# Kernel optimization log

Measured on AMD Instinct MI355X. Metric: run time of the kernel, lower is better.

Reference implementation:

```python
import jax, jax.numpy as jnp
import numpy as np

B, N, D = 2, 256, 512
H = 4 * D  # mlp_hidden_dim


def setup_inputs() -> dict:
    key = jax.random.key(0)
    ks = jax.random.split(key, 14)
    s_in = 1.0 / np.sqrt(D)
    s_h = 1.0 / np.sqrt(H)
    s_cat = 1.0 / np.sqrt(2 * D)
    return {
        "x_v": jax.random.normal(ks[0], (B, N, D), jnp.float32),
        "x_a": jax.random.normal(ks[1], (B, N, D), jnp.float32),
        # weights stored as (in, out); y = x @ W + b (same math as torch Linear)
        "W1v": jax.random.uniform(ks[2], (D, H), jnp.float32, -s_in, s_in),
        "b1v": jax.random.uniform(ks[3], (H,), jnp.float32, -s_in, s_in),
        "W1a": jax.random.uniform(ks[4], (D, H), jnp.float32, -s_in, s_in),
        "b1a": jax.random.uniform(ks[5], (H,), jnp.float32, -s_in, s_in),
        "Wmv": jax.random.uniform(ks[6], (H, D), jnp.float32, -s_h, s_h),
        "bmv": jax.random.uniform(ks[7], (D,), jnp.float32, -s_h, s_h),
        "Wma": jax.random.uniform(ks[8], (H, D), jnp.float32, -s_h, s_h),
        "bma": jax.random.uniform(ks[9], (D,), jnp.float32, -s_h, s_h),
        "Wout": jax.random.uniform(ks[10], (2 * D, D), jnp.float32, -s_cat, s_cat),
        "bout": jax.random.uniform(ks[11], (D,), jnp.float32, -s_cat, s_cat),
    }


def reference(x_v, x_a, W1v, b1v, W1a, b1a, Wmv, bmv, Wma, bma, Wout, bout):
    # pairwise Manhattan distance: [B, N, M]
    dist = jnp.sum(jnp.abs(x_v[:, :, None, :] - x_a[:, None, :, :]), axis=-1)
    dv = dist.mean(axis=2)  # [B, N] mean distance of each v-token to all a-tokens
    da = dist.mean(axis=1)  # [B, M]
    xv_w = x_v * dv[..., None]
    xa_w = x_a * da[..., None]
    # dropout prob = 0.0 -> identity
    hv = jax.nn.gelu(xv_w @ W1v + b1v, approximate=False) @ Wmv + bmv
    ha = jax.nn.gelu(xa_w @ W1a + b1a, approximate=False) @ Wma + bma
    combined = jnp.concatenate([hv, ha], axis=-1)  # [B, N, 2D]
    return combined @ Wout + bout
```

## Files before the change

kernel.cpp:

```cpp
#include <hip/hip_runtime.h>
#include <math.h>

#define Bsz  2
#define Ntok 256
#define Ddim 512
#define Hdim 2048
#define Mrows 512

typedef __bf16 bf16_8 __attribute__((ext_vector_type(8)));
typedef __bf16 bf16_4 __attribute__((ext_vector_type(4)));
typedef float  f32x4_t __attribute__((ext_vector_type(4)));

struct PrepPtrs {
    const float* src[3];
    __bf16*      dst[3];
    const float* xv;
    const float* xa;
    float*       pv;
    float*       pa;
    float*       out;
    float*       bc;
};

__global__ __launch_bounds__(256) void prep_kernel(PrepPtrs p) {
    __shared__ float tile[64][65];
    __shared__ float red[4][4];

    int blk = blockIdx.x;
    int tid = threadIdx.x;

    if (blk < 640) {
        const int Ks[3]  = {512, 512, 1024};
        const int Ns[3]  = {2048, 2048, 512};
        const int off[4] = {0, 256, 512, 640};
        int mi = 0;
        while (blk >= off[mi + 1]) ++mi;
        int local = blk - off[mi];
        int shift = (mi < 2) ? 5 : 3;
        int bx = local & ((1 << shift) - 1);
        int by = local >> shift;
        const float* src = p.src[mi];
        __bf16*      dst = p.dst[mi];
        int K = Ks[mi], N = Ns[mi];
        int n0 = bx << 6, k0 = by << 6;

        int klb = tid >> 4, nl = (tid & 15) << 2;
#pragma unroll
        for (int pass = 0; pass < 4; ++pass) {
            int kl = (pass << 4) + klb;
            float4 v = *(const float4*)&src[(size_t)(k0 + kl) * N + n0 + nl];
            tile[kl][nl + 0] = v.x;
            tile[kl][nl + 1] = v.y;
            tile[kl][nl + 2] = v.z;
            tile[kl][nl + 3] = v.w;
        }
        __syncthreads();
        int nl2 = tid >> 2, kb = (tid & 3) << 2;
#pragma unroll
        for (int pass = 0; pass < 4; ++pass) {
            int kl2 = (pass << 4) + kb;
            bf16_4 o;
#pragma unroll
            for (int i = 0; i < 4; ++i) o[i] = (__bf16)tile[kl2 + i][nl2];
            *(bf16_4*)&dst[(size_t)(n0 + nl2) * K + k0 + kl2] = o;
        }
    } else if (blk < 1664) {
        int bx   = blk - 640;
        int jc   = bx & 3;
        int g    = bx >> 2;
        int role = g >> 7;
        int b    = (g >> 6) & 1;
        int i0   = (g & 63) << 2;
        const float* Q    = role ? p.xa : p.xv;
        const float* S    = role ? p.xv : p.xa;
        float*       outp = role ? p.pa : p.pv;

        int d0 = tid << 1;
        const float* Qb = Q + ((size_t)b * Ntok + i0) * Ddim + d0;
        const float* Sb = S + ((size_t)b * Ntok + (jc << 6)) * Ddim + d0;

        float2 q[4];
#pragma unroll
        for (int r = 0; r < 4; ++r) q[r] = *(const float2*)(Qb + r * Ddim);

        float acc[4] = {0.f, 0.f, 0.f, 0.f};
#pragma unroll 4
        for (int j = 0; j < 64; ++j) {
            float2 s = *(const float2*)(Sb + (size_t)j * Ddim);
#pragma unroll
            for (int r = 0; r < 4; ++r)
                acc[r] += fabsf(q[r].x - s.x) + fabsf(q[r].y - s.y);
        }
        int lane = tid & 63, wv = tid >> 6;
#pragma unroll
        for (int r = 0; r < 4; ++r) {
            float v = acc[r];
#pragma unroll
            for (int off2 = 32; off2; off2 >>= 1) v += __shfl_down(v, off2);
            if (lane == 0) red[wv][r] = v;
        }
        __syncthreads();
        if (tid < 4) {
            float v = red[0][tid] + red[1][tid] + red[2][tid] + red[3][tid];
            outp[jc * Mrows + b * Ntok + i0 + tid] = v;
        }
    } else {
        int zb = blk - 1664;
        float4 z4 = {0.f, 0.f, 0.f, 0.f};
        *(float4*)&p.out[((size_t)zb * 256 + tid) * 4] = z4;
        if (zb == 0 && tid < 128) *(float4*)&p.bc[tid * 4] = z4;
    }
}

template <int GELU, int AMODE, int BFP32, int OUTM>
__device__ void gemm_tile(__bf16 (&As)[2][64][40], __bf16 (&Bs)[2][64][40],
                          const void* Aa, int lda, const void* Bv, int ldb,
                          const float* bias, const float* scale4,
                          void* C, int ldc, int Kdim,
                          int m0, int n0, int addBias) {
    const int tid = threadIdx.x;
    const int row = tid >> 2;
    const int kc  = (tid & 3) << 3;

    const __bf16* Bb  = (const __bf16*)Bv + (size_t)(n0 + row) * ldb + kc;
    const float*  Bf  = (const float*)Bv + (size_t)(n0 + row) * ldb + kc;
    const float*  Af  = (const float*)Aa + (size_t)(m0 + row) * lda + kc;
    const __bf16* Ab  = (const __bf16*)Aa + (size_t)(m0 + row) * lda + kc;
    float s = 1.0f;
    if (AMODE == 1) {
        int m = m0 + row;
        s = (scale4[m] + scale4[Mrows + m] + scale4[2 * Mrows + m] +
             scale4[3 * Mrows + m]) * (1.0f / 256.0f);
    }

    const int wave = tid >> 6, lane = tid & 63;
    const int moff = (wave >> 1) << 5, noff = (wave & 1) << 5;
    const int lrow = lane & 15, quad = lane >> 4;

    struct Stage {
        float4 aF0, aF1, bF0, bF1;
        bf16_8 a8, b8;
    };
    Stage sR, sN;

    auto loadStage = [&](int kt, Stage& st) {
        if (BFP32) {
            st.bF0 = *(const float4*)(Bf + kt);
            st.bF1 = *(const float4*)(Bf + kt + 4);
        } else {
            st.b8 = *(const bf16_8*)(Bb + kt);
        }
        if (AMODE == 1) {
            st.aF0 = *(const float4*)(Af + kt);
            st.aF1 = *(const float4*)(Af + kt + 4);
        } else {
            st.a8 = *(const bf16_8*)(Ab + kt);
        }
    };
    auto storeStage = [&](int buf, const Stage& st) {
        bf16_8 a8, b8;
        if (AMODE == 1) {
            a8[0] = (__bf16)(st.aF0.x * s); a8[1] = (__bf16)(st.aF0.y * s);
            a8[2] = (__bf16)(st.aF0.z * s); a8[3] = (__bf16)(st.aF0.w * s);
            a8[4] = (__bf16)(st.aF1.x * s); a8[5] = (__bf16)(st.aF1.y * s);
            a8[6] = (__bf16)(st.aF1.z * s); a8[7] = (__bf16)(st.aF1.w * s);
        } else {
            a8 = st.a8;
        }
        if (BFP32) {
            b8[0] = (__bf16)st.bF0.x; b8[1] = (__bf16)st.bF0.y;
            b8[2] = (__bf16)st.bF0.z; b8[3] = (__bf16)st.bF0.w;
            b8[4] = (__bf16)st.bF1.x; b8[5] = (__bf16)st.bF1.y;
            b8[6] = (__bf16)st.bF1.z; b8[7] = (__bf16)st.bF1.w;
        } else {
            b8 = st.b8;
        }
        *(bf16_8*)&As[buf][row][kc] = a8;
        *(bf16_8*)&Bs[buf][row][kc] = b8;
    };

    f32x4_t acc00 = {0.f, 0.f, 0.f, 0.f};
    f32x4_t acc01 = {0.f, 0.f, 0.f, 0.f};
    f32x4_t acc10 = {0.f, 0.f, 0.f, 0.f};
    f32x4_t acc11 = {0.f, 0.f, 0.f, 0.f};

    const int nIter = Kdim >> 5;

    loadStage(0, sR);
    storeStage(0, sR);
    if (nIter > 1) loadStage(32, sR);
    __syncthreads();

    for (int it = 0; it < nIter; ++it) {
        const int cur = it & 1;
        bf16_8 a0 = *(const bf16_8*)&As[cur][moff + lrow][quad << 3];
        bf16_8 a1 = *(const bf16_8*)&As[cur][moff + 16 + lrow][quad << 3];
        bf16_8 b0 = *(const bf16_8*)&Bs[cur][noff + lrow][quad << 3];
        bf16_8 b1 = *(const bf16_8*)&Bs[cur][noff + 16 + lrow][quad << 3];
        if (it + 2 < nIter) loadStage((it + 2) << 5, sN);
        acc00 = __builtin_amdgcn_mfma_f32_16x16x32_bf16(a0, b0, acc00, 0, 0, 0);
        acc01 = __builtin_amdgcn_mfma_f32_16x16x32_bf16(a0, b1, acc01, 0, 0, 0);
        acc10 = __builtin_amdgcn_mfma_f32_16x16x32_bf16(a1, b0, acc10, 0, 0, 0);
        acc11 = __builtin_amdgcn_mfma_f32_16x16x32_bf16(a1, b1, acc11, 0, 0, 0);
        if (it + 1 < nIter) {
            storeStage(cur ^ 1, sR);
            sR = sN;
            __syncthreads();
        }
    }

    f32x4_t accs[2][2] = {{acc00, acc01}, {acc10, acc11}};
#pragma unroll
    for (int ti = 0; ti < 2; ++ti) {
#pragma unroll
        for (int tj = 0; tj < 2; ++tj) {
            int colg = n0 + noff + (tj << 4) + lrow;
            float bv = addBias ? bias[colg] : 0.0f;
#pragma unroll
            for (int r = 0; r < 4; ++r) {
                int rowg = m0 + moff + (ti << 4) + (quad << 2) + r;
                float v = accs[ti][tj][r] + bv;
                if (GELU) v = 0.5f * v * (1.0f + erff(v * 0.70710678118654752f));
                if (OUTM == 1)
                    ((__bf16*)C)[(size_t)rowg * ldc + colg] = (__bf16)v;
                else
                    atomicAdd((float*)C + (size_t)rowg * ldc + colg, v);
            }
        }
    }
}

struct APtrs {
    const float*  x[2];
    const __bf16* WT1[2];
    const float*  b1[2];
    const float*  pd[2];
    __bf16*       g1[2];
    const __bf16* WTout;
    const float*  Wm[2];
    const float*  bm[2];
    const float*  Wout;
    const float*  bout;
    __bf16*       WcT[2];
    float*        bc;
};

__global__ __launch_bounds__(256) void kernelA(APtrs p) {
    __shared__ __align__(16) __bf16 As[2][64][40];
    __shared__ __align__(16) __bf16 Bs[2][64][40];
    int blk = blockIdx.x;
    if (blk < 512) {
        int z = blk >> 8, t = blk & 255;
        int mt = t >> 5, nt = t & 31;
        gemm_tile<1, 1, 0, 1>(As, Bs, p.x[z], Ddim, p.WT1[z], Ddim,
                              p.b1[z], p.pd[z], p.g1[z], Hdim, Ddim,
                              mt << 6, nt << 6, 1);
    } else if (blk < 1024) {
        int b2 = blk - 512;
        int z = b2 >> 8, t = b2 & 255;
        int mt = t >> 5, nt = t & 31;
        gemm_tile<0, 0, 1, 1>(As, Bs, p.WTout + z * 512, 2 * Ddim,
                              p.Wm[z], Ddim, nullptr, nullptr,
                              p.WcT[z], Hdim, Ddim, mt << 6, nt << 6, 0);
    } else {
        int kb = blk - 1024;
        int tid = threadIdx.x;
        float a0 = 0.f, a1 = 0.f, a2 = 0.f, a3 = 0.f;
#pragma unroll 4
        for (int kk = 0; kk < 128; kk += 2) {
            int k0 = (kb << 7) + kk, k1 = k0 + 1;
            float bk0 = (k0 < 512) ? p.bm[0][k0] : p.bm[1][k0 - 512];
            float bk1 = (k1 < 512) ? p.bm[0][k1] : p.bm[1][k1 - 512];
            a0 += bk0 * p.Wout[(size_t)k0 * Ddim + tid];
            a1 += bk0 * p.Wout[(size_t)k0 * Ddim + tid + 256];
            a2 += bk1 * p.Wout[(size_t)k1 * Ddim + tid];
            a3 += bk1 * p.Wout[(size_t)k1 * Ddim + tid + 256];
        }
        if (kb == 0) { a0 += p.bout[tid]; a1 += p.bout[tid + 256]; }
        atomicAdd(&p.bc[tid],       a0 + a2);
        atomicAdd(&p.bc[tid + 256], a1 + a3);
    }
}

struct BPtrs {
    const __bf16* g1[2];
    const __bf16* WcT[2];
    const float*  bc;
    float*        out;
};

__global__ __launch_bounds__(256) void kernelB(BPtrs p) {
    __shared__ __align__(16) __bf16 As[2][64][40];
    __shared__ __align__(16) __bf16 Bs[2][64][40];
    int nt = blockIdx.x & 7, mt = (blockIdx.x >> 3) & 7, kz = blockIdx.x >> 6;
    int z = kz >> 2, koff = (kz & 3) << 9;
    gemm_tile<0, 0, 0, 2>(As, Bs, p.g1[z] + koff, Hdim, p.WcT[z] + koff, Hdim,
                          p.bc, nullptr, p.out, Ddim, Ddim,
                          mt << 6, nt << 6, kz == 0);
}

extern "C" void kernel_launch(void* const* d_in, const int* in_sizes, int n_in,
                              void* d_out, int out_size, void* d_ws, size_t ws_size,
                              hipStream_t stream) {
    const float* x_v  = (const float*)d_in[0];
    const float* x_a  = (const float*)d_in[1];
    const float* W1v  = (const float*)d_in[2];
    const float* b1v  = (const float*)d_in[3];
    const float* W1a  = (const float*)d_in[4];
    const float* b1a  = (const float*)d_in[5];
    const float* Wmv  = (const float*)d_in[6];
    const float* bmv  = (const float*)d_in[7];
    const float* Wma  = (const float*)d_in[8];
    const float* bma  = (const float*)d_in[9];
    const float* Wout = (const float*)d_in[10];
    const float* bout = (const float*)d_in[11];
    float* out = (float*)d_out;

    char* w = (char*)d_ws;
    auto alloc = [&](size_t bytes) {
        char* r = w;
        w += (bytes + 255) & ~(size_t)255;
        return (void*)r;
    };
    float*    pv    = (float*)alloc(4 * Mrows * 4);
    float*    pa    = (float*)alloc(4 * Mrows * 4);
    float*    bc    = (float*)alloc(Ddim * 4);
    __bf16*   WT1v  = (__bf16*)alloc((size_t)Hdim * Ddim * 2);
    __bf16*   WT1a  = (__bf16*)alloc((size_t)Hdim * Ddim * 2);
    __bf16*   WTout = (__bf16*)alloc((size_t)Ddim * 2 * Ddim * 2);
    __bf16*   WcTv  = (__bf16*)alloc((size_t)Ddim * Hdim * 2);
    __bf16*   WcTa  = (__bf16*)alloc((size_t)Ddim * Hdim * 2);
    __bf16*   g1v   = (__bf16*)alloc((size_t)Mrows * Hdim * 2);
    __bf16*   g1a   = (__bf16*)alloc((size_t)Mrows * Hdim * 2);

    PrepPtrs pp;
    pp.src[0] = W1v;  pp.dst[0] = WT1v;
    pp.src[1] = W1a;  pp.dst[1] = WT1a;
    pp.src[2] = Wout; pp.dst[2] = WTout;
    pp.xv = x_v; pp.xa = x_a; pp.pv = pv; pp.pa = pa;
    pp.out = out; pp.bc = bc;
    prep_kernel<<<dim3(1920), dim3(256), 0, stream>>>(pp);

    APtrs ap;
    ap.x[0] = x_v; ap.x[1] = x_a;
    ap.WT1[0] = WT1v; ap.WT1[1] = WT1a;
    ap.b1[0] = b1v; ap.b1[1] = b1a;
    ap.pd[0] = pv; ap.pd[1] = pa;
    ap.g1[0] = g1v; ap.g1[1] = g1a;
    ap.WTout = WTout;
    ap.Wm[0] = Wmv; ap.Wm[1] = Wma;
    ap.bm[0] = bmv; ap.bm[1] = bma;
    ap.Wout = Wout; ap.bout = bout;
    ap.WcT[0] = WcTv; ap.WcT[1] = WcTa;
    ap.bc = bc;
    kernelA<<<dim3(1032), dim3(256), 0, stream>>>(ap);

    BPtrs bp;
    bp.g1[0] = g1v; bp.g1[1] = g1a;
    bp.WcT[0] = WcTv; bp.WcT[1] = WcTa;
    bp.bc = bc; bp.out = out;
    kernelB<<<dim3(512), dim3(256), 0, stream>>>(bp);
}
```

Before: 130.6 us.

## Pre-convert activations to bf16 in prep and move bias-combine into prep kernel

The distance blocks now also write bf16 copies of x_v and x_a, so the first GEMM in kernelA loads bf16 activations and rescales them in registers instead of loading fp32. The bias-combine computation (bm·Wout + bout) moves from kernelA into prep_kernel, and zeroing of out and bc moves to hipMemsetAsync calls. This halves the activation bytes read by the first GEMM and shortens kernelA, at the cost of an extra bf16 round-trip, two memset launches, and scaling applied after bf16 rounding. Prep must complete the bc atomics after the memset, which stream order guarantees.

Measured after the change: 129.0 us. Within noise of the previous version (-1.2%).

```diff
diff --git a/kernel.cpp b/kernel.cpp
--- a/kernel.cpp
+++ b/kernel.cpp
@@ -9,6 +9,7 @@
 
 typedef __bf16 bf16_8 __attribute__((ext_vector_type(8)));
 typedef __bf16 bf16_4 __attribute__((ext_vector_type(4)));
+typedef __bf16 bf16_2 __attribute__((ext_vector_type(2)));
 typedef float  f32x4_t __attribute__((ext_vector_type(4)));
 
 struct PrepPtrs {
@@ -16,9 +17,12 @@
     __bf16*      dst[3];
     const float* xv;
     const float* xa;
+    __bf16*      xbf[2];
     float*       pv;
     float*       pa;
-    float*       out;
+    const float* bm[2];
+    const float* Wout;
+    const float* bout;
     float*       bc;
 };
 
@@ -83,6 +87,17 @@
 #pragma unroll
         for (int r = 0; r < 4; ++r) q[r] = *(const float2*)(Qb + r * Ddim);
 
+        if (jc == 0) {
+            __bf16* xb = p.xbf[role];
+#pragma unroll
+            for (int r = 0; r < 4; ++r) {
+                bf16_2 o;
+                o[0] = (__bf16)q[r].x;
+                o[1] = (__bf16)q[r].y;
+                *(bf16_2*)&xb[((size_t)b * Ntok + i0 + r) * Ddim + d0] = o;
+            }
+        }
+
         float acc[4] = {0.f, 0.f, 0.f, 0.f};
 #pragma unroll 4
         for (int j = 0; j < 64; ++j) {
@@ -105,10 +120,21 @@
             outp[jc * Mrows + b * Ntok + i0 + tid] = v;
         }
     } else {
-        int zb = blk - 1664;
-        float4 z4 = {0.f, 0.f, 0.f, 0.f};
-        *(float4*)&p.out[((size_t)zb * 256 + tid) * 4] = z4;
-        if (zb == 0 && tid < 128) *(float4*)&p.bc[tid * 4] = z4;
+        int kb = blk - 1664;
+        float a0 = 0.f, a1 = 0.f, a2 = 0.f, a3 = 0.f;
+#pragma unroll 4
+        for (int kk = 0; kk < 128; kk += 2) {
+            int k0 = (kb << 7) + kk, k1 = k0 + 1;
+            float bk0 = (k0 < 512) ? p.bm[0][k0] : p.bm[1][k0 - 512];
+            float bk1 = (k1 < 512) ? p.bm[0][k1] : p.bm[1][k1 - 512];
+            a0 += bk0 * p.Wout[(size_t)k0 * Ddim + tid];
+            a1 += bk0 * p.Wout[(size_t)k0 * Ddim + tid + 256];
+            a2 += bk1 * p.Wout[(size_t)k1 * Ddim + tid];
+            a3 += bk1 * p.Wout[(size_t)k1 * Ddim + tid + 256];
+        }
+        if (kb == 0) { a0 += p.bout[tid]; a1 += p.bout[tid + 256]; }
+        atomicAdd(&p.bc[tid],       a0 + a2);
+        atomicAdd(&p.bc[tid + 256], a1 + a3);
     }
 }
 
@@ -127,7 +153,7 @@
     const float*  Af  = (const float*)Aa + (size_t)(m0 + row) * lda + kc;
     const __bf16* Ab  = (const __bf16*)Aa + (size_t)(m0 + row) * lda + kc;
     float s = 1.0f;
-    if (AMODE == 1) {
+    if (AMODE == 1 || AMODE == 3) {
         int m = m0 + row;
         s = (scale4[m] + scale4[Mrows + m] + scale4[2 * Mrows + m] +
              scale4[3 * Mrows + m]) * (1.0f / 256.0f);
@@ -164,6 +190,10 @@
             a8[2] = (__bf16)(st.aF0.z * s); a8[3] = (__bf16)(st.aF0.w * s);
             a8[4] = (__bf16)(st.aF1.x * s); a8[5] = (__bf16)(st.aF1.y * s);
             a8[6] = (__bf16)(st.aF1.z * s); a8[7] = (__bf16)(st.aF1.w * s);
+        } else if (AMODE == 3) {
+#pragma unroll
+            for (int i = 0; i < 8; ++i)
+                a8[i] = (__bf16)((float)st.a8[i] * s);
         } else {
             a8 = st.a8;
         }
@@ -231,18 +261,14 @@
 }
 
 struct APtrs {
-    const float*  x[2];
+    const __bf16* xbf[2];
     const __bf16* WT1[2];
     const float*  b1[2];
     const float*  pd[2];
     __bf16*       g1[2];
     const __bf16* WTout;
     const float*  Wm[2];
-    const float*  bm[2];
-    const float*  Wout;
-    const float*  bout;
     __bf16*       WcT[2];
-    float*        bc;
 };
 
 __global__ __launch_bounds__(256) void kernelA(APtrs p) {
@@ -252,33 +278,16 @@
     if (blk < 512) {
         int z = blk >> 8, t = blk & 255;
         int mt = t >> 5, nt = t & 31;
-        gemm_tile<1, 1, 0, 1>(As, Bs, p.x[z], Ddim, p.WT1[z], Ddim,
+        gemm_tile<1, 3, 0, 1>(As, Bs, p.xbf[z], Ddim, p.WT1[z], Ddim,
                               p.b1[z], p.pd[z], p.g1[z], Hdim, Ddim,
                               mt << 6, nt << 6, 1);
-    } else if (blk < 1024) {
+    } else {
         int b2 = blk - 512;
         int z = b2 >> 8, t = b2 & 255;
         int mt = t >> 5, nt = t & 31;
         gemm_tile<0, 0, 1, 1>(As, Bs, p.WTout + z * 512, 2 * Ddim,
                               p.Wm[z], Ddim, nullptr, nullptr,
                               p.WcT[z], Hdim, Ddim, mt << 6, nt << 6, 0);
-    } else {
-        int kb = blk - 1024;
-        int tid = threadIdx.x;
-        float a0 = 0.f, a1 = 0.f, a2 = 0.f, a3 = 0.f;
-#pragma unroll 4
-        for (int kk = 0; kk < 128; kk += 2) {
-            int k0 = (kb << 7) + kk, k1 = k0 + 1;
-            float bk0 = (k0 < 512) ? p.bm[0][k0] : p.bm[1][k0 - 512];
-            float bk1 = (k1 < 512) ? p.bm[0][k1] : p.bm[1][k1 - 512];
-            a0 += bk0 * p.Wout[(size_t)k0 * Ddim + tid];
-            a1 += bk0 * p.Wout[(size_t)k0 * Ddim + tid + 256];
-            a2 += bk1 * p.Wout[(size_t)k1 * Ddim + tid];
-            a3 += bk1 * p.Wout[(size_t)k1 * Ddim + tid + 256];
-        }
-        if (kb == 0) { a0 += p.bout[tid]; a1 += p.bout[tid + 256]; }
-        atomicAdd(&p.bc[tid],       a0 + a2);
-        atomicAdd(&p.bc[tid + 256], a1 + a3);
     }
 }
 
@@ -325,6 +334,8 @@
     float*    pv    = (float*)alloc(4 * Mrows * 4);
     float*    pa    = (float*)alloc(4 * Mrows * 4);
     float*    bc    = (float*)alloc(Ddim * 4);
+    __bf16*   xbfv  = (__bf16*)alloc((size_t)Mrows * Ddim * 2);
+    __bf16*   xbfa  = (__bf16*)alloc((size_t)Mrows * Ddim * 2);
     __bf16*   WT1v  = (__bf16*)alloc((size_t)Hdim * Ddim * 2);
     __bf16*   WT1a  = (__bf16*)alloc((size_t)Hdim * Ddim * 2);
     __bf16*   WTout = (__bf16*)alloc((size_t)Ddim * 2 * Ddim * 2);
@@ -333,27 +344,31 @@
     __bf16*   g1v   = (__bf16*)alloc((size_t)Mrows * Hdim * 2);
     __bf16*   g1a   = (__bf16*)alloc((size_t)Mrows * Hdim * 2);
 
+    hipMemsetAsync(out, 0, (size_t)Mrows * Ddim * 4, stream);
+    hipMemsetAsync(bc, 0, Ddim * 4, stream);
+
     PrepPtrs pp;
     pp.src[0] = W1v;  pp.dst[0] = WT1v;
     pp.src[1] = W1a;  pp.dst[1] = WT1a;
     pp.src[2] = Wout; pp.dst[2] = WTout;
-    pp.xv = x_v; pp.xa = x_a; pp.pv = pv; pp.pa = pa;
-    pp.out = out; pp.bc = bc;
-    prep_kernel<<<dim3(1920), dim3(256), 0, stream>>>(pp);
+    pp.xv = x_v; pp.xa = x_a;
+    pp.xbf[0] = xbfv; pp.xbf[1] = xbfa;
+    pp.pv = pv; pp.pa = pa;
+    pp.bm[0] = bmv; pp.bm[1] = bma;
+    pp.Wout = Wout; pp.bout = bout;
+    pp.bc = bc;
+    prep_kernel<<<dim3(1672), dim3(256), 0, stream>>>(pp);
 
     APtrs ap;
-    ap.x[0] = x_v; ap.x[1] = x_a;
+    ap.xbf[0] = xbfv; ap.xbf[1] = xbfa;
     ap.WT1[0] = WT1v; ap.WT1[1] = WT1a;
     ap.b1[0] = b1v; ap.b1[1] = b1a;
     ap.pd[0] = pv; ap.pd[1] = pa;
     ap.g1[0] = g1v; ap.g1[1] = g1a;
     ap.WTout = WTout;
     ap.Wm[0] = Wmv; ap.Wm[1] = Wma;
-    ap.bm[0] = bmv; ap.bm[1] = bma;
-    ap.Wout = Wout; ap.bout = bout;
     ap.WcT[0] = WcTv; ap.WcT[1] = WcTa;
-    ap.bc = bc;
-    kernelA<<<dim3(1032), dim3(256), 0, stream>>>(ap);
+    kernelA<<<dim3(1024), dim3(256), 0, stream>>>(ap);
 
     BPtrs bp;
     bp.g1[0] = g1v; bp.g1[1] = g1a;
```
